# Kernel tuning notes

Hardware: AMD Instinct MI355X
Metric: run time of the kernel (lower is better)

## Reference

```python
import jax, jax.numpy as jnp
from jax import lax
import numpy as np

B, S, T = 256, 1024, 96  # batch, seq_len, tag_size (incl. <BOS>, <EOS>)
START_TAG, STOP_TAG = T - 2, T - 1


def setup_inputs() -> dict:
    key = jax.random.key(0)
    k1, k2, k3, k4 = jax.random.split(key, 4)
    features = jax.random.normal(k1, (B, S, T), dtype=jnp.float32)
    lengths = jax.random.randint(k2, (B,), S // 2, S + 1)
    mask = (jnp.arange(S)[None, :] < lengths[:, None])  # (B,S) bool, prefix mask
    y = jax.random.randint(k3, (B, S), 0, START_TAG).astype(jnp.int64)  # real tags only
    transitions = jax.random.normal(k4, (T, T), dtype=jnp.float32) * 0.1
    return {"features": features, "mask": mask, "y": y, "transitions": transitions}


def _crf_nll(features, mask, y, transitions):
    Bv, Sv, Tv = features.shape
    # ---- log Z via forward algorithm (scan over time) ----
    # scores[t,b,i,j] = features[b,t,j] + transitions[i,j]
    part0 = features[:, 0, :] + transitions[START_TAG, :]  # (B,T) = scores[0,:,START,:]
    feats_t = jnp.swapaxes(features, 0, 1)  # (S,B,T)
    mask_t = jnp.swapaxes(mask, 0, 1)       # (S,B)

    def step(part, inp):
        f_t, m_t = inp  # (B,T), (B,)
        # tmp[b,i,j] = f_t[b,j] + transitions[i,j] + part[b,i]
        tmp = f_t[:, None, :] + transitions[None, :, :] + part[:, :, None]
        new_part = jax.nn.logsumexp(tmp, axis=1)  # (B,T)
        part = jnp.where(m_t[:, None], new_part, part)
        return part, None

    part, _ = lax.scan(step, part0, (feats_t[1:], mask_t[1:]))
    # final transition to STOP, take STOP column of logsumexp over i
    logZ = jnp.sum(jax.nn.logsumexp(part + transitions[:, STOP_TAG][None, :], axis=1))

    # ---- gold score ----
    prev = jnp.concatenate(
        [jnp.full((Bv, 1), START_TAG, dtype=y.dtype), y[:, :-1]], axis=1)  # (B,S)
    emit = jnp.take_along_axis(features, y[:, :, None], axis=2)[:, :, 0]  # features[b,t,y]
    trans = transitions[prev, y]                                          # transitions[prev,y]
    tgt_energy = jnp.sum(jnp.where(mask, emit + trans, 0.0))
    lengths = mask.sum(axis=1)
    last_tag = jnp.take_along_axis(y, (lengths - 1)[:, None], axis=1)[:, 0]
    end_energy = jnp.sum(transitions[last_tag, STOP_TAG])
    gold_score = tgt_energy + end_energy
    return logZ - gold_score


def reference(features, mask, y, transitions):
    return _crf_nll(features, mask, y, transitions)
```

## Files before the change

### kernel.cpp

```cpp
#include <hip/hip_runtime.h>
#include <stdint.h>

#define TT 96
#define SS 1024
#define BB 256
#define START_TAG 94
#define STOP_TAG 95
#define LOG2E 1.44269504088896340736f
#define LN2   0.69314718055994530942f

typedef float f32x2 __attribute__((ext_vector_type(2)));
typedef float f32x4v __attribute__((ext_vector_type(4)));
typedef __bf16 bf16x8 __attribute__((ext_vector_type(8)));

#define EF_BYTES   50331648u
#define ABUF_OFF   50331648u
#define ESTART_OFF 50350080u
#define ESTOP_OFF  50356224u
#define WS_NEED    50427904u

union U4B { uint4 u; bf16x8 v; };

static __device__ __forceinline__ uint32_t pk_bf16(float a, float b) {
    uint32_t r;
    asm("v_cvt_pk_bf16_f32 %0, %1, %2" : "=v"(r) : "v"(a), "v"(b));
    return r;
}
static __device__ __forceinline__ f32x2 pmax2(f32x2 a, f32x2 b) {
#if __has_builtin(__builtin_elementwise_max)
    return __builtin_elementwise_max(a, b);
#else
    f32x2 r; r.x = fmaxf(a.x, b.x); r.y = fmaxf(a.y, b.y); return r;
#endif
}

#define MFMA(a, b, c) __builtin_amdgcn_mfma_f32_16x16x32_bf16((a), (b), (c), 0, 0, 0)
#define GLD(srcp, dstp) __builtin_amdgcn_global_load_lds( \
    (const __attribute__((address_space(1))) uint32_t*)(srcp), \
    (__attribute__((address_space(3))) uint32_t*)(dstp), 16, 0, 0)

__global__ __launch_bounds__(256) void prep_consts(const float* __restrict__ tr,
                                                   char* __restrict__ ws) {
    int i = blockIdx.x * 256 + threadIdx.x;
    if (i < 4608) {
        uint32_t* A = (uint32_t*)(ws + ABUF_OFF);
        int tile = i >> 8, rem = i & 255, l = rem >> 2, v = rem & 3;
        int mt = tile / 3, kt = tile - mt * 3;
        int hi = l >> 4, m = 16 * mt + (l & 15);
        int k0 = 32 * kt + 16 * (v >> 1) + 4 * hi + 2 * (v & 1);
        A[i] = pk_bf16(expf(tr[k0 * TT + m]), expf(tr[(k0 + 1) * TT + m]));
    } else if (i < 4608 + 2 * 1536) {
        int e = i - 4608;
        int stop = (e >= 1536) ? 1 : 0;
        if (stop) e -= 1536;
        int l = e / 24, c = e % 24;
        int mt = c >> 2, r = c & 3, hi = l >> 4;
        int j = 16 * mt + 4 * hi + r;
        float* dst = (float*)(ws + (stop ? ESTOP_OFF : ESTART_OFF));
        dst[e] = expf(stop ? tr[j * TT + STOP_TAG] : tr[START_TAG * TT + j]);
    }
}

__global__ __launch_bounds__(256) void ef_kernel2(const float* __restrict__ f,
                                                  uint32_t* __restrict__ ef) {
    int tid = blockIdx.x * 256 + threadIdx.x;
    int p   = tid % 6;
    int r   = tid / 6;
    int l   = r & 63;
    int bt  = r >> 6;
    int t   = bt & 1023;
    int blk = bt >> 10;
    int b   = blk * 16 + (l & 15);
    int hi  = l >> 4;
    const float4* fp = (const float4*)(f + (size_t)(b * SS + t) * TT + 16 * p + 4 * hi);
    float4 v = *fp;
    uint2 w;
    w.x = pk_bf16(expf(v.x), expf(v.y));
    w.y = pk_bf16(expf(v.z), expf(v.w));
    *(uint2*)(ef + (size_t)r * 12 + 2 * p) = w;
}

__global__ __launch_bounds__(64, 1) void fwd_kernel(
    const float* __restrict__ features, const int* __restrict__ mask,
    const int* __restrict__ y, const float* __restrict__ trans,
    const char* __restrict__ ws, float* __restrict__ out)
{
    const int l = threadIdx.x;

    if (blockIdx.x >= 16) {
        int bg = blockIdx.x - 16;
        float e = 0.f;
        #pragma unroll 1
        for (int k = 0; k < 18; ++k) {
            int idx = bg * 64 + l + k * 15360;
            if (idx < BB * SS) {
                int t = idx & (SS - 1);
                if (mask[idx]) {
                    int yt   = y[idx];
                    int prev = t ? y[idx - 1] : START_TAG;
                    e += features[(size_t)idx * TT + yt] + trans[prev * TT + yt];
                    bool last = (t == SS - 1) || (mask[idx + 1] == 0);
                    if (last) e += trans[yt * TT + STOP_TAG];
                }
            }
        }
        #pragma unroll
        for (int d = 1; d < 64; d <<= 1) e += __shfl_xor(e, d);
        if (l == 0) atomicAdd(out, -e);
        return;
    }

    __shared__ __align__(16) char ring[16 * 3072];
    char* ringc = (char*)ring;

    const int blk = blockIdx.x;
    const int n = l & 15;

    int cnt = 0;
    {
        const int4* mrow = (const int4*)(mask + (blk * 16 + n) * SS + 512 + (l >> 4) * 128);
        #pragma unroll
        for (int k = 0; k < 32; ++k) {
            int4 mv = mrow[k];
            cnt += mv.x + mv.y + mv.z + mv.w;
        }
        cnt += __shfl_xor(cnt, 16);
        cnt += __shfl_xor(cnt, 32);
    }
    const int len_m1 = cnt + 512 - 1;

    bf16x8 Af[6][3];
    {
        const uint4* ab = (const uint4*)(ws + ABUF_OFF);
        #pragma unroll
        for (int mt = 0; mt < 6; ++mt)
            #pragma unroll
            for (int kt = 0; kt < 3; ++kt) {
                U4B ub; ub.u = ab[(mt * 3 + kt) * 64 + l];
                Af[mt][kt] = ub.v;
            }
    }
    f32x2 estL[6], estH[6];
    {
        const float4* es1 = (const float4*)(ws + ESTOP_OFF);
        #pragma unroll
        for (int mt = 0; mt < 6; ++mt) {
            float4 v = es1[l * 6 + mt];
            estL[mt].x = v.x; estL[mt].y = v.y;
            estH[mt].x = v.z; estH[mt].y = v.w;
        }
    }
    f32x2 esrL[6], esrH[6];
    {
        const float4* es0 = (const float4*)(ws + ESTART_OFF);
        #pragma unroll
        for (int mt = 0; mt < 6; ++mt) {
            float4 v = es0[l * 6 + mt];
            esrL[mt].x = v.x; esrL[mt].y = v.y;
            esrH[mt].x = v.z; esrH[mt].y = v.w;
        }
    }

    const char* efg = ws + (size_t)blk * SS * 3072 + l * 16;
    #pragma unroll
    for (int s = 0; s < 8; ++s) {
        const char* sp = efg + s * 3072;
        char* dp = ringc + s * 3072;
        GLD(sp, dp); GLD(sp + 1024, dp + 1024); GLD(sp + 2048, dp + 2048);
    }
    asm volatile("s_waitcnt vmcnt(0)" ::: "memory");

    uint4 PA[3], PB[3];
    {
        const uint4* rp = (const uint4*)(ringc + l * 48);
        PA[0] = rp[0]; PA[1] = rp[1]; PA[2] = rp[2];
        const uint4* rq = (const uint4*)(ringc + 3072 + l * 48);
        PB[0] = rq[0]; PB[1] = rq[1]; PB[2] = rq[2];
    }

    float c2 = 0.f, pe = 0.f, logz = 0.f;
    f32x2 pend2; pend2.x = 1.f; pend2.y = 1.f;
    bf16x8 Bf[3];
    const f32x4v Z4 = {0.f, 0.f, 0.f, 0.f};

#define UNPACKP(PBUF, EFP) { \
    uint32_t w_[12] = { PBUF[0].x, PBUF[0].y, PBUF[0].z, PBUF[0].w, \
                        PBUF[1].x, PBUF[1].y, PBUF[1].z, PBUF[1].w, \
                        PBUF[2].x, PBUF[2].y, PBUF[2].z, PBUF[2].w }; \
    _Pragma("unroll") \
    for (int q_ = 0; q_ < 12; ++q_) { \
        EFP[q_ >> 1][q_ & 1].x = __uint_as_float(w_[q_] << 16); \
        EFP[q_ >> 1][q_ & 1].y = __uint_as_float(w_[q_] & 0xffff0000u); \
    } }

#define PACKB2(AFL, AFH) { \
    uint32_t wlo_[6], whi_[6]; \
    _Pragma("unroll") \
    for (int mt_ = 0; mt_ < 6; ++mt_) { \
        wlo_[mt_] = pk_bf16(AFL[mt_].x, AFL[mt_].y); \
        whi_[mt_] = pk_bf16(AFH[mt_].x, AFH[mt_].y); } \
    _Pragma("unroll") \
    for (int kt_ = 0; kt_ < 3; ++kt_) { \
        U4B ub_; ub_.u.x = wlo_[2 * kt_]; ub_.u.y = whi_[2 * kt_]; \
        ub_.u.z = wlo_[2 * kt_ + 1]; ub_.u.w = whi_[2 * kt_ + 1]; \
        Bf[kt_] = ub_.v; } }

    {
        {
            const char* sp = efg + 8 * 3072;
            char* dp = ringc + 8 * 3072;
            GLD(sp, dp); GLD(sp + 1024, dp + 1024); GLD(sp + 2048, dp + 2048);
        }
        f32x2 efp[6][2];
        UNPACKP(PA, efp);
        f32x2 afL[6], afH[6];
        #pragma unroll
        for (int mt = 0; mt < 6; ++mt) {
            afL[mt] = efp[mt][0] * esrL[mt];
            afH[mt] = efp[mt][1] * esrH[mt];
        }
        PACKB2(afL, afH);
        asm volatile("s_waitcnt vmcnt(18)" ::: "memory");
        const uint4* rp = (const uint4*)(ringc + 2 * 3072 + l * 48);
        PA[0] = rp[0]; PA[1] = rp[1]; PA[2] = rp[2];
    }

#define STEP(PBUF, TCUR, APPLY, ARED) { \
    const int t_ = (TCUR); \
    { int ts_ = t_ + 8; if (ts_ > 1023) ts_ = 1023; \
      const char* sp_ = efg + (size_t)ts_ * 3072; \
      char* dp_ = ringc + ((t_ + 8) & 15) * 3072; \
      GLD(sp_, dp_); GLD(sp_ + 1024, dp_ + 1024); GLD(sp_ + 2048, dp_ + 2048); } \
    f32x4v acc[6]; \
    _Pragma("unroll") \
    for (int mt_ = 0; mt_ < 6; ++mt_) { \
        acc[mt_] = MFMA(Af[mt_][0], Bf[0], Z4); \
        acc[mt_] = MFMA(Af[mt_][1], Bf[1], acc[mt_]); \
        acc[mt_] = MFMA(Af[mt_][2], Bf[2], acc[mt_]); } \
    f32x2 efp[6][2]; \
    UNPACKP(PBUF, efp); \
    f32x2 afL[6], afH[6]; \
    _Pragma("unroll") \
    for (int mt_ = 0; mt_ < 6; ++mt_) { \
        f32x2 aL_, aH_; \
        aL_.x = acc[mt_][0]; aL_.y = acc[mt_][1]; \
        aH_.x = acc[mt_][2]; aH_.y = acc[mt_][3]; \
        if (APPLY) { aL_ = aL_ * pend2; aH_ = aH_ * pend2; } \
        afL[mt_] = aL_ * efp[mt_][0]; \
        afH[mt_] = aH_ * efp[mt_][1]; } \
    if (APPLY) { c2 += pe; } \
    asm volatile("s_waitcnt vmcnt(18)" ::: "memory"); \
    { const uint4* rp_ = (const uint4*)(ringc + ((t_ + 2) & 15) * 3072 + l * 48); \
      PBUF[0] = rp_[0]; PBUF[1] = rp_[1]; PBUF[2] = rp_[2]; } \
    PACKB2(afL, afH); \
    { int cap_ = (len_m1 == t_); \
      if (__any(cap_)) { \
          f32x2 ds_ = afL[0] * estL[0]; \
          ds_ = ds_ + afH[0] * estH[0]; \
          _Pragma("unroll") \
          for (int mt_ = 1; mt_ < 6; ++mt_) { \
              ds_ = ds_ + afL[mt_] * estL[mt_]; \
              ds_ = ds_ + afH[mt_] * estH[mt_]; } \
          float dd_ = ds_.x + ds_.y; \
          dd_ += __shfl_xor(dd_, 16); dd_ += __shfl_xor(dd_, 32); \
          float lz_ = LN2 * (c2 + log2f(dd_)); \
          logz = cap_ ? lz_ : logz; } } \
    if (ARED) { \
        f32x2 mp_ = pmax2(afL[0], afH[0]); \
        _Pragma("unroll") \
        for (int mt_ = 1; mt_ < 6; ++mt_) \
            mp_ = pmax2(mp_, pmax2(afL[mt_], afH[mt_])); \
        float mm_ = fmaxf(mp_.x, mp_.y); \
        mm_ = fmaxf(mm_, __shfl_xor(mm_, 16)); \
        mm_ = fmaxf(mm_, __shfl_xor(mm_, 32)); \
        unsigned eb_ = (__float_as_uint(mm_) >> 23) & 255u; \
        pe = (float)((int)eb_ - 127); \
        float pn_ = __uint_as_float((254u - eb_) << 23); \
        pend2.x = pn_; pend2.y = pn_; } }

    STEP(PB, 1, 1, 0)
    STEP(PA, 2, 0, 0)
    STEP(PB, 3, 0, 1)
    #pragma unroll 1
    for (int tb = 1; tb < 256; ++tb) {
        const int t4 = tb * 4;
        STEP(PA, t4 + 0, 0, 0)
        STEP(PB, t4 + 1, 1, 0)
        STEP(PA, t4 + 2, 0, 0)
        STEP(PB, t4 + 3, 0, 1)
    }

    if (l < 16) atomicAdd(out, logz);
#undef STEP
#undef PACKB2
#undef UNPACKP
}

__global__ void fb_prep(const float* __restrict__ trans, float* __restrict__ E2T) {
    int idx = blockIdx.x * blockDim.x + threadIdx.x;
    if (idx < TT * TT) {
        int jj = idx / TT, ii = idx % TT;
        E2T[idx] = expf(trans[ii * TT + jj]);
    }
}

__global__ __launch_bounds__(384) void fb_forward(
    const float* __restrict__ features, const int* __restrict__ mask,
    const float* __restrict__ trans, const float* __restrict__ E2T,
    float* __restrict__ out)
{
    const int b    = blockIdx.x;
    const int tid  = threadIdx.x;
    const int j    = tid >> 2;
    const int q    = tid & 3;
    const int lane = tid & 63;
    const int wv   = tid >> 6;

    __shared__ float alpha[2][TT];
    __shared__ float fch[2][16 * TT];
    __shared__ float wred[6];
    __shared__ int   wcnt[6];
    __shared__ int   len_sh;

    int cnt = 0;
    for (int i = tid; i < SS; i += 384) cnt += (mask[b * SS + i] != 0);
    #pragma unroll
    for (int d = 1; d < 64; d <<= 1) cnt += __shfl_xor(cnt, d);
    if (lane == 0) wcnt[wv] = cnt;
    __syncthreads();
    if (tid == 0) {
        int L = 0;
        for (int w = 0; w < 6; ++w) L += wcnt[w];
        len_sh = L;
    }

    float Er[24];
    {
        const float4* ep = reinterpret_cast<const float4*>(E2T + j * TT + q * 24);
        #pragma unroll
        for (int k = 0; k < 6; ++k) {
            float4 e4 = ep[k];
            Er[4*k+0] = e4.x; Er[4*k+1] = e4.y; Er[4*k+2] = e4.z; Er[4*k+3] = e4.w;
        }
    }

    const float* fb = features + (size_t)b * SS * TT;
    float4 r0    = reinterpret_cast<const float4*>(fb)[tid];
    float4 rnext = reinterpret_cast<const float4*>(fb + 16 * TT)[tid];
    reinterpret_cast<float4*>(&fch[0][0])[tid] = r0;
    __syncthreads();
    const int len = len_sh;

    if (q == 0) {
        float p0 = fch[0][j] + trans[START_TAG * TT + j];
        alpha[0][j] = exp2f(p0 * LOG2E);
    }
    __syncthreads();

    float c2 = 0.0f;
    float pending = 1.0f;
    int   pe = 0;

    const int clast = (len - 1) >> 4;
    for (int c = 0; c <= clast; ++c) {
        if (c > 0) {
            reinterpret_cast<float4*>(&fch[c & 1][0])[tid] = rnext;
            int cn = c + 1; if (cn > SS / 16 - 1) cn = SS / 16 - 1;
            rnext = reinterpret_cast<const float4*>(fb + cn * 16 * TT)[tid];
            __syncthreads();
        }
        const int t0   = c * 16;
        const int tbeg = (c == 0) ? 1 : t0;
        int tend = t0 + 16; if (tend > len) tend = len;

        for (int t = tbeg; t < tend; ++t) {
            const float* acur = alpha[(t + 1) & 1];
            const float4* ap = reinterpret_cast<const float4*>(acur + q * 24);
            float sum = 0.0f;
            #pragma unroll
            for (int k = 0; k < 6; ++k) {
                float4 a = ap[k];
                sum = fmaf(Er[4*k+0], a.x, sum);
                sum = fmaf(Er[4*k+1], a.y, sum);
                sum = fmaf(Er[4*k+2], a.z, sum);
                sum = fmaf(Er[4*k+3], a.w, sum);
            }
            sum += __shfl_xor(sum, 1);
            sum += __shfl_xor(sum, 2);

            float f    = fch[c & 1][(t - t0) * TT + j];
            float anew = sum * exp2f(f * LOG2E) * pending;
            c2 += (float)pe; pe = 0; pending = 1.0f;

            if (q == 0) alpha[t & 1][j] = anew;
            if ((t & 3) == 3) {
                float m = anew;
                m = fmaxf(m, __shfl_xor(m, 4));
                m = fmaxf(m, __shfl_xor(m, 8));
                m = fmaxf(m, __shfl_xor(m, 16));
                m = fmaxf(m, __shfl_xor(m, 32));
                if (lane == 0) wred[wv] = m;
            }
            __syncthreads();
            if ((t & 3) == 3) {
                float mv = wred[0];
                #pragma unroll
                for (int w = 1; w < 6; ++w) mv = fmaxf(mv, wred[w]);
                int eb  = (int)((__float_as_uint(mv) >> 23) & 255u);
                pe      = eb - 127;
                pending = __uint_as_float((uint32_t)(254 - eb) << 23);
            }
        }
    }

    float v = 0.0f;
    if (q == 0) v = alpha[(len - 1) & 1][j] * E2T[STOP_TAG * TT + j];
    #pragma unroll
    for (int d = 1; d < 64; d <<= 1) v += __shfl_xor(v, d);
    __syncthreads();
    if (lane == 0) wred[wv] = v;
    __syncthreads();
    if (tid == 0) {
        float tot = 0.0f;
        for (int w = 0; w < 6; ++w) tot += wred[w];
        atomicAdd(out, LN2 * (c2 + log2f(tot)));
    }
}

__global__ void fb_gold(const float* __restrict__ features, const int* __restrict__ mask,
                        const int* __restrict__ y, const float* __restrict__ trans,
                        float* __restrict__ out)
{
    int idx = blockIdx.x * blockDim.x + threadIdx.x;
    float e = 0.0f;
    if (idx < BB * SS) {
        int t = idx % SS;
        if (mask[idx] != 0) {
            int yt   = y[idx];
            int prev = (t == 0) ? START_TAG : y[idx - 1];
            e = features[(size_t)idx * TT + yt] + trans[prev * TT + yt];
            bool is_last = (t == SS - 1) || (mask[idx + 1] == 0);
            if (is_last) e += trans[yt * TT + STOP_TAG];
        }
    }
    #pragma unroll
    for (int d = 1; d < 64; d <<= 1) e += __shfl_xor(e, d);
    __shared__ float ws4[4];
    int lane = threadIdx.x & 63, wv = threadIdx.x >> 6;
    if (lane == 0) ws4[wv] = e;
    __syncthreads();
    if (threadIdx.x == 0) {
        float s = ws4[0] + ws4[1] + ws4[2] + ws4[3];
        atomicAdd(out, -s);
    }
}

extern "C" void kernel_launch(void* const* d_in, const int* in_sizes, int n_in,
                              void* d_out, int out_size, void* d_ws, size_t ws_size,
                              hipStream_t stream) {
    const float* features = (const float*)d_in[0];
    const int*   mask     = (const int*)d_in[1];
    const int*   y        = (const int*)d_in[2];
    const float* trans    = (const float*)d_in[3];
    float*       out      = (float*)d_out;

    hipMemsetAsync(d_out, 0, sizeof(float) * out_size, stream);

    if (ws_size >= WS_NEED) {
        char* ws = (char*)d_ws;
        prep_consts<<<30, 256, 0, stream>>>(trans, ws);
        ef_kernel2<<<24576, 256, 0, stream>>>(features, (uint32_t*)ws);
        fwd_kernel<<<256, 64, 0, stream>>>(features, mask, y, trans, ws, out);
    } else {
        float* E2T = (float*)d_ws;
        fb_prep<<<(TT * TT + 255) / 256, 256, 0, stream>>>(trans, E2T);
        fb_forward<<<BB, 384, 0, stream>>>(features, mask, trans, E2T, out);
        fb_gold<<<(BB * SS) / 256, 256, 0, stream>>>(features, mask, y, trans, out);
    }
}
```

Measured before the change: 538.9 us.

## Interleave four independent batch chains per wavefront in CRF forward kernel

```diff
diff --git a/kernel.cpp b/kernel.cpp
--- a/kernel.cpp
+++ b/kernel.cpp
@@ -87,12 +87,12 @@
 {
     const int l = threadIdx.x;
 
-    if (blockIdx.x >= 16) {
-        int bg = blockIdx.x - 16;
+    if (blockIdx.x >= 4) {
+        int bg = blockIdx.x - 4;
         float e = 0.f;
         #pragma unroll 1
-        for (int k = 0; k < 18; ++k) {
-            int idx = bg * 64 + l + k * 15360;
+        for (int k = 0; k < 17; ++k) {
+            int idx = bg * 64 + l + k * 16128;
             if (idx < BB * SS) {
                 int t = idx & (SS - 1);
                 if (mask[idx]) {
@@ -110,15 +110,17 @@
         return;
     }
 
-    __shared__ __align__(16) char ring[16 * 3072];
+    __shared__ __align__(16) char ring[4 * 8 * 3072];
     char* ringc = (char*)ring;
 
-    const int blk = blockIdx.x;
-    const int n = l & 15;
-
-    int cnt = 0;
-    {
-        const int4* mrow = (const int4*)(mask + (blk * 16 + n) * SS + 512 + (l >> 4) * 128);
+    const int blk4 = blockIdx.x * 4;
+    const int n = l & 15, hi = l >> 4;
+
+    int len_m1[4];
+    #pragma unroll
+    for (int c = 0; c < 4; ++c) {
+        int cnt = 0;
+        const int4* mrow = (const int4*)(mask + ((blk4 + c) * 16 + n) * SS + 512 + hi * 128);
         #pragma unroll
         for (int k = 0; k < 32; ++k) {
             int4 mv = mrow[k];
@@ -126,8 +128,8 @@
         }
         cnt += __shfl_xor(cnt, 16);
         cnt += __shfl_xor(cnt, 32);
-    }
-    const int len_m1 = cnt + 512 - 1;
+        len_m1[c] = cnt + 511;
+    }
 
     bf16x8 Af[6][3];
     {
@@ -150,37 +152,26 @@
             estH[mt].x = v.z; estH[mt].y = v.w;
         }
     }
-    f32x2 esrL[6], esrH[6];
-    {
-        const float4* es0 = (const float4*)(ws + ESTART_OFF);
-        #pragma unroll
-        for (int mt = 0; mt < 6; ++mt) {
-            float4 v = es0[l * 6 + mt];
-            esrL[mt].x = v.x; esrL[mt].y = v.y;
-            esrH[mt].x = v.z; esrH[mt].y = v.w;
-        }
-    }
-
-    const char* efg = ws + (size_t)blk * SS * 3072 + l * 16;
-    #pragma unroll
-    for (int s = 0; s < 8; ++s) {
-        const char* sp = efg + s * 3072;
-        char* dp = ringc + s * 3072;
-        GLD(sp, dp); GLD(sp + 1024, dp + 1024); GLD(sp + 2048, dp + 2048);
-    }
+
+    const char* efg[4];
+    #pragma unroll
+    for (int c = 0; c < 4; ++c)
+        efg[c] = ws + (size_t)(blk4 + c) * SS * 3072 + l * 16;
+
+    #pragma unroll
+    for (int s = 0; s < 4; ++s)
+        #pragma unroll
+        for (int c = 0; c < 4; ++c) {
+            const char* sp = efg[c] + s * 3072;
+            char* dp = ringc + c * 24576 + s * 3072;
+            GLD(sp, dp); GLD(sp + 1024, dp + 1024); GLD(sp + 2048, dp + 2048);
+        }
     asm volatile("s_waitcnt vmcnt(0)" ::: "memory");
 
-    uint4 PA[3], PB[3];
-    {
-        const uint4* rp = (const uint4*)(ringc + l * 48);
-        PA[0] = rp[0]; PA[1] = rp[1]; PA[2] = rp[2];
-        const uint4* rq = (const uint4*)(ringc + 3072 + l * 48);
-        PB[0] = rq[0]; PB[1] = rq[1]; PB[2] = rq[2];
-    }
-
-    float c2 = 0.f, pe = 0.f, logz = 0.f;
-    f32x2 pend2; pend2.x = 1.f; pend2.y = 1.f;
-    bf16x8 Bf[3];
+    float c2[4], pe[4], logz[4];
+    f32x2 pend2[4];
+    bf16x8 Bf[4][3];
+    uint4 PA[4][3];
     const f32x4v Z4 = {0.f, 0.f, 0.f, 0.f};
 
 #define UNPACKP(PBUF, EFP) { \
@@ -193,7 +184,7 @@
         EFP[q_ >> 1][q_ & 1].y = __uint_as_float(w_[q_] & 0xffff0000u); \
     } }
 
-#define PACKB2(AFL, AFH) { \
+#define PACKB2(AFL, AFH, BDST) { \
     uint32_t wlo_[6], whi_[6]; \
     _Pragma("unroll") \
     for (int mt_ = 0; mt_ < 6; ++mt_) { \
@@ -203,95 +194,111 @@
     for (int kt_ = 0; kt_ < 3; ++kt_) { \
         U4B ub_; ub_.u.x = wlo_[2 * kt_]; ub_.u.y = whi_[2 * kt_]; \
         ub_.u.z = wlo_[2 * kt_ + 1]; ub_.u.w = whi_[2 * kt_ + 1]; \
-        Bf[kt_] = ub_.v; } }
+        BDST[kt_] = ub_.v; } }
 
     {
-        {
-            const char* sp = efg + 8 * 3072;
-            char* dp = ringc + 8 * 3072;
-            GLD(sp, dp); GLD(sp + 1024, dp + 1024); GLD(sp + 2048, dp + 2048);
-        }
-        f32x2 efp[6][2];
-        UNPACKP(PA, efp);
-        f32x2 afL[6], afH[6];
+        f32x2 esrL[6], esrH[6];
+        const float4* es0 = (const float4*)(ws + ESTART_OFF);
         #pragma unroll
         for (int mt = 0; mt < 6; ++mt) {
-            afL[mt] = efp[mt][0] * esrL[mt];
-            afH[mt] = efp[mt][1] * esrH[mt];
-        }
-        PACKB2(afL, afH);
-        asm volatile("s_waitcnt vmcnt(18)" ::: "memory");
-        const uint4* rp = (const uint4*)(ringc + 2 * 3072 + l * 48);
-        PA[0] = rp[0]; PA[1] = rp[1]; PA[2] = rp[2];
-    }
-
-#define STEP(PBUF, TCUR, APPLY, ARED) { \
-    const int t_ = (TCUR); \
-    { int ts_ = t_ + 8; if (ts_ > 1023) ts_ = 1023; \
-      const char* sp_ = efg + (size_t)ts_ * 3072; \
-      char* dp_ = ringc + ((t_ + 8) & 15) * 3072; \
-      GLD(sp_, dp_); GLD(sp_ + 1024, dp_ + 1024); GLD(sp_ + 2048, dp_ + 2048); } \
-    f32x4v acc[6]; \
+            float4 v = es0[l * 6 + mt];
+            esrL[mt].x = v.x; esrL[mt].y = v.y;
+            esrH[mt].x = v.z; esrH[mt].y = v.w;
+        }
+        #pragma unroll
+        for (int c = 0; c < 4; ++c) {
+            uint4 T[3];
+            const uint4* rp = (const uint4*)(ringc + c * 24576 + l * 48);
+            T[0] = rp[0]; T[1] = rp[1]; T[2] = rp[2];
+            f32x2 efp[6][2];
+            UNPACKP(T, efp);
+            f32x2 afL[6], afH[6];
+            #pragma unroll
+            for (int mt = 0; mt < 6; ++mt) {
+                afL[mt] = efp[mt][0] * esrL[mt];
+                afH[mt] = efp[mt][1] * esrH[mt];
+            }
+            PACKB2(afL, afH, Bf[c]);
+            const uint4* rq = (const uint4*)(ringc + c * 24576 + 3072 + l * 48);
+            PA[c][0] = rq[0]; PA[c][1] = rq[1]; PA[c][2] = rq[2];
+            c2[c] = 0.f; pe[c] = 0.f; logz[c] = 0.f;
+            pend2[c].x = 1.f; pend2[c].y = 1.f;
+        }
+    }
+
+#define SUPER(T, APPLY, ARED) { \
+    const int t_ = (T); \
+    { int ts_ = t_ + 3; if (ts_ > 1023) ts_ = 1023; \
+      _Pragma("unroll") \
+      for (int c_ = 0; c_ < 4; ++c_) { \
+          const char* sp_ = efg[c_] + (size_t)ts_ * 3072; \
+          char* dp_ = ringc + c_ * 24576 + ((t_ + 3) & 7) * 3072; \
+          GLD(sp_, dp_); GLD(sp_ + 1024, dp_ + 1024); GLD(sp_ + 2048, dp_ + 2048); } } \
+    asm volatile("s_waitcnt vmcnt(24)" ::: "memory"); \
     _Pragma("unroll") \
-    for (int mt_ = 0; mt_ < 6; ++mt_) { \
-        acc[mt_] = MFMA(Af[mt_][0], Bf[0], Z4); \
-        acc[mt_] = MFMA(Af[mt_][1], Bf[1], acc[mt_]); \
-        acc[mt_] = MFMA(Af[mt_][2], Bf[2], acc[mt_]); } \
-    f32x2 efp[6][2]; \
-    UNPACKP(PBUF, efp); \
-    f32x2 afL[6], afH[6]; \
-    _Pragma("unroll") \
-    for (int mt_ = 0; mt_ < 6; ++mt_) { \
-        f32x2 aL_, aH_; \
-        aL_.x = acc[mt_][0]; aL_.y = acc[mt_][1]; \
-        aH_.x = acc[mt_][2]; aH_.y = acc[mt_][3]; \
-        if (APPLY) { aL_ = aL_ * pend2; aH_ = aH_ * pend2; } \
-        afL[mt_] = aL_ * efp[mt_][0]; \
-        afH[mt_] = aH_ * efp[mt_][1]; } \
-    if (APPLY) { c2 += pe; } \
-    asm volatile("s_waitcnt vmcnt(18)" ::: "memory"); \
-    { const uint4* rp_ = (const uint4*)(ringc + ((t_ + 2) & 15) * 3072 + l * 48); \
-      PBUF[0] = rp_[0]; PBUF[1] = rp_[1]; PBUF[2] = rp_[2]; } \
-    PACKB2(afL, afH); \
-    { int cap_ = (len_m1 == t_); \
-      if (__any(cap_)) { \
-          f32x2 ds_ = afL[0] * estL[0]; \
-          ds_ = ds_ + afH[0] * estH[0]; \
-          _Pragma("unroll") \
-          for (int mt_ = 1; mt_ < 6; ++mt_) { \
-              ds_ = ds_ + afL[mt_] * estL[mt_]; \
-              ds_ = ds_ + afH[mt_] * estH[mt_]; } \
-          float dd_ = ds_.x + ds_.y; \
-          dd_ += __shfl_xor(dd_, 16); dd_ += __shfl_xor(dd_, 32); \
-          float lz_ = LN2 * (c2 + log2f(dd_)); \
-          logz = cap_ ? lz_ : logz; } } \
-    if (ARED) { \
-        f32x2 mp_ = pmax2(afL[0], afH[0]); \
+    for (int c_ = 0; c_ < 4; ++c_) { \
+        f32x4v acc[6]; \
         _Pragma("unroll") \
-        for (int mt_ = 1; mt_ < 6; ++mt_) \
-            mp_ = pmax2(mp_, pmax2(afL[mt_], afH[mt_])); \
-        float mm_ = fmaxf(mp_.x, mp_.y); \
-        mm_ = fmaxf(mm_, __shfl_xor(mm_, 16)); \
-        mm_ = fmaxf(mm_, __shfl_xor(mm_, 32)); \
-        unsigned eb_ = (__float_as_uint(mm_) >> 23) & 255u; \
-        pe = (float)((int)eb_ - 127); \
-        float pn_ = __uint_as_float((254u - eb_) << 23); \
-        pend2.x = pn_; pend2.y = pn_; } }
-
-    STEP(PB, 1, 1, 0)
-    STEP(PA, 2, 0, 0)
-    STEP(PB, 3, 0, 1)
+        for (int mt_ = 0; mt_ < 6; ++mt_) { \
+            acc[mt_] = MFMA(Af[mt_][0], Bf[c_][0], Z4); \
+            acc[mt_] = MFMA(Af[mt_][1], Bf[c_][1], acc[mt_]); \
+            acc[mt_] = MFMA(Af[mt_][2], Bf[c_][2], acc[mt_]); } \
+        f32x2 efp[6][2]; \
+        UNPACKP(PA[c_], efp); \
+        f32x2 afL[6], afH[6]; \
+        _Pragma("unroll") \
+        for (int mt_ = 0; mt_ < 6; ++mt_) { \
+            f32x2 aL_, aH_; \
+            aL_.x = acc[mt_][0]; aL_.y = acc[mt_][1]; \
+            aH_.x = acc[mt_][2]; aH_.y = acc[mt_][3]; \
+            if (APPLY) { aL_ = aL_ * pend2[c_]; aH_ = aH_ * pend2[c_]; } \
+            afL[mt_] = aL_ * efp[mt_][0]; \
+            afH[mt_] = aH_ * efp[mt_][1]; } \
+        if (APPLY) { c2[c_] += pe[c_]; } \
+        { const uint4* rp_ = (const uint4*)(ringc + c_ * 24576 + ((t_ + 1) & 7) * 3072 + l * 48); \
+          PA[c_][0] = rp_[0]; PA[c_][1] = rp_[1]; PA[c_][2] = rp_[2]; } \
+        PACKB2(afL, afH, Bf[c_]); \
+        { int cap_ = (len_m1[c_] == t_); \
+          if (__any(cap_)) { \
+              f32x2 ds_ = afL[0] * estL[0]; \
+              ds_ = ds_ + afH[0] * estH[0]; \
+              _Pragma("unroll") \
+              for (int mt_ = 1; mt_ < 6; ++mt_) { \
+                  ds_ = ds_ + afL[mt_] * estL[mt_]; \
+                  ds_ = ds_ + afH[mt_] * estH[mt_]; } \
+              float dd_ = ds_.x + ds_.y; \
+              dd_ += __shfl_xor(dd_, 16); dd_ += __shfl_xor(dd_, 32); \
+              float lz_ = LN2 * (c2[c_] + log2f(dd_)); \
+              logz[c_] = cap_ ? lz_ : logz[c_]; } } \
+        if (ARED) { \
+            f32x2 mp_ = pmax2(afL[0], afH[0]); \
+            _Pragma("unroll") \
+            for (int mt_ = 1; mt_ < 6; ++mt_) \
+                mp_ = pmax2(mp_, pmax2(afL[mt_], afH[mt_])); \
+            float mm_ = fmaxf(mp_.x, mp_.y); \
+            mm_ = fmaxf(mm_, __shfl_xor(mm_, 16)); \
+            mm_ = fmaxf(mm_, __shfl_xor(mm_, 32)); \
+            unsigned eb_ = (__float_as_uint(mm_) >> 23) & 255u; \
+            pe[c_] = (float)((int)eb_ - 127); \
+            float pn_ = __uint_as_float((254u - eb_) << 23); \
+            pend2[c_].x = pn_; pend2[c_].y = pn_; } \
+    } }
+
+    SUPER(1, 1, 0)
+    SUPER(2, 0, 0)
+    SUPER(3, 0, 1)
     #pragma unroll 1
     for (int tb = 1; tb < 256; ++tb) {
         const int t4 = tb * 4;
-        STEP(PA, t4 + 0, 0, 0)
-        STEP(PB, t4 + 1, 1, 0)
-        STEP(PA, t4 + 2, 0, 0)
-        STEP(PB, t4 + 3, 0, 1)
-    }
-
-    if (l < 16) atomicAdd(out, logz);
-#undef STEP
+        SUPER(t4 + 0, 0, 0)
+        SUPER(t4 + 1, 1, 0)
+        SUPER(t4 + 2, 0, 0)
+        SUPER(t4 + 3, 0, 1)
+    }
+
+    float s = logz[0] + logz[1] + logz[2] + logz[3];
+    if (l < 16) atomicAdd(out, s);
+#undef SUPER
 #undef PACKB2
 #undef UNPACKP
 }
```

Result: slower. 1.542 ms (+186.1%).
